# Kernel optimization log

Measured on AMD Instinct MI355X. Metric: run time of the kernel, lower is better.

Reference implementation:

```python
import jax, jax.numpy as jnp
import numpy as np

N, E, R = 100000, 600000, 2      # nodes, edges per relation, relations
IN, H, DH = 128, 8, 16           # input dim, heads, per-head hidden
D = H * DH                       # 128 = hidden_dim * n_heads
RIN, RH = 64, 16                 # relation input / hidden dims
SLOPE = 0.2                      # leaky relu negative slope


def _leaky(v):
    return jnp.where(v >= 0, v, SLOPE * v)


def setup_inputs() -> dict:
    key = jax.random.key(0)
    ks = jax.random.split(key, 18)
    nrm = lambda k, shape, s: jax.random.normal(k, shape, jnp.float32) * s
    sc = 1.0 / np.sqrt(D).astype(np.float32)
    return {
        'x': nrm(ks[0], (N, IN), 1.0),
        'src': jax.random.randint(ks[1], (R, E), 0, N, jnp.int32),
        'dst': jax.random.randint(ks[2], (R, E), 0, N, jnp.int32),
        'rel_emb': nrm(ks[3], (R, RIN), 1.0),
        'Wp': nrm(ks[4], (IN, D), sc), 'bp': jnp.zeros((D,), jnp.float32),
        'Wn': nrm(ks[5], (D, D), sc), 'bn': jnp.zeros((D,), jnp.float32),
        'Wsrc': nrm(ks[6], (R, D, D), sc), 'bsrc': jnp.zeros((R, D), jnp.float32),
        'Wrel': nrm(ks[7], (R, RIN, H * 2 * DH), 1.0 / np.sqrt(RIN).astype(np.float32)),
        'resW': nrm(ks[8], (IN, D), sc), 'resb': jnp.zeros((D,), jnp.float32),
        'res_alpha': nrm(ks[9], (1,), 1.0),
        'crossW': nrm(ks[10], (R, H, DH), 1.0 / np.sqrt(DH).astype(np.float32)),
        'Wprop': nrm(ks[11], (R, RIN, H * RH), 1.0 / np.sqrt(RIN).astype(np.float32)),
        'bprop': jnp.zeros((R, H * RH), jnp.float32),
    }


def reference(x, src, dst, rel_emb, Wp, bp, Wn, bn, Wsrc, bsrc, Wrel,
              resW, resb, res_alpha, crossW, Wprop, bprop):
    # projection_layer (R_HGT) then node_transformation_layers (layer input transform)
    xp = x @ Wp + bp                                  # [N, D]
    h = (xp @ Wn + bn).reshape(N, H, DH)              # [N, H, DH] dst-side features
    res = (xp @ resW + resb).reshape(N, H, DH)        # res_fc(input_dst)

    def per_rel(sr, dr, e_emb, Ws, bs, Wr):
        # relation_src_node_transformation + relation-conditioned attention
        s = (h.reshape(N, D) @ Ws + bs).reshape(N, H, DH)   # src messages
        a = (e_emb @ Wr).reshape(H, 2, DH)                  # relation attn vectors
        sc_src = (s * a[:, 0]).sum(-1)                      # [N, H]
        sc_dst = (h * a[:, 1]).sum(-1)                      # [N, H]
        e_sc = _leaky(sc_src[sr] + sc_dst[dr])              # [E, H]
        # edge softmax over incoming edges of each dst node
        m = jax.lax.stop_gradient(jax.ops.segment_max(e_sc, dr, num_segments=N))
        ex = jnp.exp(e_sc - m[dr])
        den = jax.ops.segment_sum(ex, dr, num_segments=N)
        alpha = ex / den[dr]                                # [E, H]
        msg = alpha[:, :, None] * s[sr]                     # [E, H, DH]
        return jax.ops.segment_sum(msg, dr, num_segments=N)  # [N, H, DH]

    out = jax.vmap(per_rel)(src, dst, rel_emb, Wsrc, bsrc, Wrel)  # [R, N, H, DH]

    # sigmoid-gated residual (shared per dst ntype)
    g = jax.nn.sigmoid(res_alpha)[0]
    out = out * g + res[None] * (1.0 - g)

    # RelationCrossing: attention across the R relation-specific dst features
    def cross(cw):
        attn = jax.nn.softmax(_leaky((out * cw[None, None]).sum(-1)), axis=0)  # [R,N,H]
        return (attn[..., None] * out).sum(0)                                  # [N,H,DH]

    fused = jax.vmap(cross)(crossW).reshape(R, N, D)      # [R, N, D]

    # relation_propagation_layer
    rel_out = jnp.einsum('ri,rio->ro', rel_emb, Wprop) + bprop  # [R, H*RH]
    return fused, rel_out
```

## Files before the change

kernel.cpp:

```cpp
#include <hip/hip_runtime.h>
#include <math.h>

#define NN 100000
#define EE 600000
#define RR 2
#define DD 128
#define HH 8
#define DHH 16
#define RN (RR * NN)
#define NT 26
#define MTOT 6250
#define NB3 ((MTOT + 3) / 4)
#define CHUNK 4096
#define NCH ((EE + CHUNK - 1) / CHUNK)
#define BINW 512
#define NBIN ((NN + BINW - 1) / BINW)
#define BCAPD 4096

typedef unsigned short ushort_t;
typedef short bf16x8 __attribute__((ext_vector_type(8)));
typedef float f32x4 __attribute__((ext_vector_type(4)));
typedef unsigned short u16x4 __attribute__((ext_vector_type(4)));

__device__ __forceinline__ float lrelu(float v) { return v >= 0.f ? v : 0.2f * v; }

__device__ __forceinline__ ushort_t f2bf(float f) {
    unsigned int u = __float_as_uint(f);
    u = (u + 0x7FFFu + ((u >> 16) & 1u)) >> 16;
    return (ushort_t)u;
}
__device__ __forceinline__ float bf2f(ushort_t u) {
    return __uint_as_float(((unsigned int)u) << 16);
}

__global__ __launch_bounds__(128) void k_compose1(
    const float* __restrict__ Wp, const float* __restrict__ bp,
    const float* __restrict__ Wn, const float* __restrict__ bn,
    const float* __restrict__ resW, const float* __restrict__ resb,
    const float* __restrict__ rel_emb, const float* __restrict__ Wrel,
    const float* __restrict__ Wprop, const float* __restrict__ bprop,
    float* __restrict__ Wpn, float* __restrict__ bpn,
    float* __restrict__ Wres_c, float* __restrict__ bres_c,
    float* __restrict__ avec, float* __restrict__ rel_out) {
    __shared__ float row[DD];
    const int rrow = blockIdx.x, tid = threadIdx.x;
    row[tid] = Wp[rrow * DD + tid];
    __syncthreads();
    float acc1 = 0.f, acc2 = 0.f;
    for (int k = 0; k < DD; ++k) {
        float wv = row[k];
        acc1 = fmaf(wv, Wn[k * DD + tid], acc1);
        acc2 = fmaf(wv, resW[k * DD + tid], acc2);
    }
    Wpn[rrow * DD + tid] = acc1;
    Wres_c[rrow * DD + tid] = acc2;
    if (rrow == 0) {
        float b1 = 0.f, b2 = 0.f;
        for (int k = 0; k < DD; ++k) {
            b1 = fmaf(bp[k], Wn[k * DD + tid], b1);
            b2 = fmaf(bp[k], resW[k * DD + tid], b2);
        }
        bpn[tid] = b1 + bn[tid];
        bres_c[tid] = b2 + resb[tid];
    }
    if (rrow < 4) {
        int idx = rrow * DD + tid;
        int r = idx >> 8, o = idx & 255;
        float acc = 0.f;
        for (int i = 0; i < 64; ++i)
            acc += rel_emb[r * 64 + i] * Wrel[(r * 64 + i) * 256 + o];
        avec[idx] = acc;
    } else if (rrow < 6) {
        int o = (rrow - 4) * DD + tid;
        int r = o >> 7, oo = o & 127;
        float acc = bprop[o];
        for (int i = 0; i < 64; ++i)
            acc += rel_emb[r * 64 + i] * Wprop[(r * 64 + i) * 128 + oo];
        rel_out[o] = acc;
    }
}

__global__ __launch_bounds__(128) void k_compose2(
    const float* __restrict__ Wpn, const float* __restrict__ bpn,
    const float* __restrict__ Wsrc, const float* __restrict__ bsrc,
    const float* __restrict__ avec,
    float* __restrict__ Ws_c, float* __restrict__ bs_c,
    float* __restrict__ VdstT, float* __restrict__ cdst) {
    __shared__ float row[DD];
    const int rel = blockIdx.x, rrow = blockIdx.y, tid = threadIdx.x;
    row[tid] = Wpn[rrow * DD + tid];
    __syncthreads();
    const float* W = Wsrc + (size_t)rel * DD * DD;
    float acc = 0.f;
    for (int k = 0; k < DD; ++k) acc = fmaf(row[k], W[k * DD + tid], acc);
    Ws_c[(size_t)rel * DD * DD + rrow * DD + tid] = acc;
    if (tid < HH) {
        float v = 0.f;
        for (int d = 0; d < 16; ++d)
            v += row[tid * 16 + d] * avec[rel * 256 + tid * 32 + 16 + d];
        VdstT[(rel * HH + tid) * DD + rrow] = v;
    }
    if (rrow == 0) {
        float b = 0.f;
        for (int k = 0; k < DD; ++k) b = fmaf(bpn[k], W[k * DD + tid], b);
        bs_c[rel * DD + tid] = b + bsrc[rel * DD + tid];
        if (rel == 0 && tid < 16) {
            int r2 = tid >> 3, h2 = tid & 7;
            float c2 = 0.f;
            for (int d = 0; d < 16; ++d)
                c2 += bpn[h2 * 16 + d] * avec[r2 * 256 + h2 * 32 + 16 + d];
            cdst[tid] = c2;
        }
    }
}

__global__ __launch_bounds__(256) void k_pack(
    const float* __restrict__ Ws_c, const float* __restrict__ Wres_c,
    const float* __restrict__ VdstT, const float* __restrict__ avec,
    const float* __restrict__ bs_c, short* __restrict__ Wpk,
    float* __restrict__ csrc) {
    const int t = blockIdx.x;
    const int kt = threadIdx.x >> 6;
    const int l = threadIdx.x & 63;
    const int c16 = l & 15;
    bf16x8 v;
    #pragma unroll
    for (int j = 0; j < 8; ++j) {
        int k = kt * 32 + (l >> 4) * 8 + j;
        float f;
        if (t < 24) {
            int m = t >> 3;
            int col = (t & 7) * 16 + c16;
            const float* W = (m == 0) ? Ws_c : (m == 1) ? Ws_c + DD * DD : Wres_c;
            f = W[k * DD + col];
        } else if (t == 24) {
            f = VdstT[c16 * DD + k];
        } else {
            int rel = c16 >> 3, h = c16 & 7;
            f = 0.f;
            for (int d = 0; d < 16; ++d)
                f += Ws_c[(size_t)rel * DD * DD + k * DD + h * 16 + d]
                     * avec[rel * 256 + h * 32 + d];
        }
        v[j] = (short)f2bf(f);
    }
    *(bf16x8*)(Wpk + ((size_t)(t * 4 + kt) * 64 + l) * 8) = v;
    if (t == 25 && threadIdx.x < 16) {
        int rel = threadIdx.x >> 3, h = threadIdx.x & 7;
        float c = 0.f;
        for (int d = 0; d < 16; ++d)
            c += bs_c[rel * DD + h * 16 + d] * avec[rel * 256 + h * 32 + d];
        csrc[threadIdx.x] = c;
    }
}

__global__ __launch_bounds__(256) void k_node3(
    const float* __restrict__ x, const short* __restrict__ Wpk,
    const float* __restrict__ bs_c, const float* __restrict__ bres_c,
    const float* __restrict__ cdst, const float* __restrict__ csrc,
    const int* __restrict__ dst, int* __restrict__ binct,
    ushort_t* __restrict__ s_out, ushort_t* __restrict__ res_out,
    float* __restrict__ sc_src, float* __restrict__ sc_dst) {
    if (blockIdx.x >= NB3) {
        __shared__ int bins[NBIN];
        const int b = blockIdx.x - NB3;
        const int rel = b / NCH, blk = b - rel * NCH;
        const int tid = threadIdx.x;
        if (tid < NBIN) bins[tid] = 0;
        __syncthreads();
        for (int i = tid; i < CHUNK; i += 256) {
            int e = blk * CHUNK + i;
            if (e < EE)
                atomicAdd(&bins[__builtin_nontemporal_load(dst + rel * EE + e) >> 9], 1);
        }
        __syncthreads();
        if (tid < NBIN) binct[((rel * NCH) + blk) * NBIN + tid] = bins[tid];
        return;
    }
    const int tid = threadIdx.x;
    const int l = tid & 63;
    const int w = tid >> 6;
    const int m16 = l & 15, g4 = l >> 4;
    const int mt = blockIdx.x * 4 + w;
    const bool live = (mt < MTOT);
    const int nb = (live ? mt : MTOT - 1) * 16;

    bf16x8 af[4];
    const float* xrow = x + (size_t)(nb + m16) * DD + g4 * 8;
    #pragma unroll
    for (int kt = 0; kt < 4; ++kt) {
        float4 v0 = *(const float4*)(xrow + kt * 32);
        float4 v1 = *(const float4*)(xrow + kt * 32 + 4);
        af[kt][0] = (short)f2bf(v0.x); af[kt][1] = (short)f2bf(v0.y);
        af[kt][2] = (short)f2bf(v0.z); af[kt][3] = (short)f2bf(v0.w);
        af[kt][4] = (short)f2bf(v1.x); af[kt][5] = (short)f2bf(v1.y);
        af[kt][6] = (short)f2bf(v1.z); af[kt][7] = (short)f2bf(v1.w);
    }

    for (int t = 0; t < NT; ++t) {
        f32x4 acc = {0.f, 0.f, 0.f, 0.f};
        #pragma unroll
        for (int kt = 0; kt < 4; ++kt) {
            bf16x8 b = *(const bf16x8*)(Wpk + ((size_t)(t * 4 + kt) * 64 + l) * 8);
            acc = __builtin_amdgcn_mfma_f32_16x16x32_bf16(af[kt], b, acc, 0, 0, 0);
        }
        if (!live) continue;
        if (t < 16) {
            const int rel = t >> 3, head = t & 7;
            const float bb = bs_c[rel * DD + head * 16 + m16];
            #pragma unroll
            for (int r = 0; r < 4; ++r) {
                const int node = nb + g4 * 4 + r;
                s_out[((size_t)rel * NN + node) * DD + head * 16 + m16] =
                    f2bf(acc[r] + bb);
            }
        } else if (t < 24) {
            const int col = (t - 16) * 16 + m16;
            const float bb = bres_c[col];
            #pragma unroll
            for (int r = 0; r < 4; ++r) {
                const int node = nb + g4 * 4 + r;
                res_out[(size_t)node * DD + col] = f2bf(acc[r] + bb);
            }
        } else if (t == 24) {
            const int rel = m16 >> 3, head = m16 & 7;
            const float bb = cdst[m16];
            #pragma unroll
            for (int r = 0; r < 4; ++r) {
                const int node = nb + g4 * 4 + r;
                sc_dst[((size_t)rel * NN + node) * HH + head] = acc[r] + bb;
            }
        } else {
            const int rel = m16 >> 3, head = m16 & 7;
            const float bb = csrc[m16];
            #pragma unroll
            for (int r = 0; r < 4; ++r) {
                const int node = nb + g4 * 4 + r;
                sc_src[((size_t)rel * NN + node) * HH + head] = acc[r] + bb;
            }
        }
    }
}

__global__ __launch_bounds__(512) void k_binscan(const int* __restrict__ binct,
                                                 int* __restrict__ runoff,
                                                 int* __restrict__ binstart,
                                                 int* __restrict__ row_ptr) {
    __shared__ int tot[512];
    const int t = threadIdx.x;
    int run = 0;
    if (t < RR * NBIN) {
        const int rel = t / NBIN, bin = t - rel * NBIN;
        for (int blk = 0; blk < NCH; ++blk) {
            int idx = ((rel * NCH) + blk) * NBIN + bin;
            int v = binct[idx];
            runoff[idx] = run;
            run += v;
        }
    }
    tot[t] = (t < RR * NBIN) ? run : 0;
    __syncthreads();
    for (int off = 1; off < 512; off <<= 1) {
        int v = (t >= off) ? tot[t - off] : 0;
        __syncthreads();
        tot[t] += v;
        __syncthreads();
    }
    if (t < RR * NBIN) binstart[t] = tot[t] - run;
    if (t == 0) {
        binstart[RR * NBIN] = RR * EE;
        row_ptr[RN] = RR * EE;
    }
}

__global__ __launch_bounds__(256) void k_binfill(
    const int* __restrict__ src, const int* __restrict__ dst,
    const int* __restrict__ runoff, const int* __restrict__ binstart,
    int* __restrict__ ebuf) {
    __shared__ int ofs[NBIN];
    __shared__ int bins[NBIN];
    const int blk = blockIdx.x, rel = blockIdx.y, tid = threadIdx.x;
    if (tid < NBIN) {
        ofs[tid] = binstart[rel * NBIN + tid] + runoff[((rel * NCH) + blk) * NBIN + tid];
        bins[tid] = 0;
    }
    __syncthreads();
    for (int i = tid; i < CHUNK; i += 256) {
        int e = blk * CHUNK + i;
        if (e < EE) {
            int d = __builtin_nontemporal_load(dst + rel * EE + e);
            int b = d >> 9;
            int loc = atomicAdd(&bins[b], 1);
            ebuf[ofs[b] + loc] =
                ((d & 511) << 17) | __builtin_nontemporal_load(src + rel * EE + e);
        }
    }
}

__global__ __launch_bounds__(256) void k_binfin(
    const int* __restrict__ ebuf, const int* __restrict__ binstart,
    int* __restrict__ row_ptr, int* __restrict__ esrc) {
    __shared__ int keys[BCAPD];
    __shared__ int cnt[BINW];
    __shared__ int scn[BINW];
    __shared__ int part[256];
    const int bin = blockIdx.x, rel = blockIdx.y, tid = threadIdx.x;
    const int p0 = binstart[rel * NBIN + bin];
    const int p1 = binstart[rel * NBIN + bin + 1];
    const int cntE = p1 - p0;
    const bool inlds = (cntE <= BCAPD);
    const int n0 = bin * BINW;
    const int nw = min(BINW, NN - n0);

    cnt[2 * tid] = 0; cnt[2 * tid + 1] = 0;
    __syncthreads();
    for (int i = tid; i < cntE; i += 256) {
        int k = __builtin_nontemporal_load(ebuf + p0 + i);
        if (inlds) keys[i] = k;
        atomicAdd(&cnt[k >> 17], 1);
    }
    __syncthreads();
    int a = cnt[2 * tid], b = cnt[2 * tid + 1];
    part[tid] = a + b;
    __syncthreads();
    for (int off = 1; off < 256; off <<= 1) {
        int v = (tid >= off) ? part[tid - off] : 0;
        __syncthreads();
        part[tid] += v;
        __syncthreads();
    }
    int excl = (tid == 0) ? 0 : part[tid - 1];
    scn[2 * tid] = excl;
    scn[2 * tid + 1] = excl + a;
    cnt[2 * tid] = 0; cnt[2 * tid + 1] = 0;
    __syncthreads();
    for (int n = tid; n < nw; n += 256)
        row_ptr[rel * NN + n0 + n] = p0 + scn[n];
    for (int i = tid; i < cntE; i += 256) {
        int k = inlds ? keys[i] : ebuf[p0 + i];
        int low = k >> 17;
        int slot = atomicAdd(&cnt[low], 1);
        esrc[p0 + scn[low] + slot] = k & 0x1FFFF;
    }
}

__global__ __launch_bounds__(256) void k_gather_cross(
    const int* __restrict__ esrc, const int* __restrict__ row_ptr,
    const float* __restrict__ sc_src, const float* __restrict__ sc_dst,
    const ushort_t* __restrict__ s, const ushort_t* __restrict__ res_buf,
    const float* __restrict__ res_alpha, const float* __restrict__ crossW,
    float* __restrict__ out) {
    int n = blockIdx.x * 4 + (threadIdx.x >> 6);
    if (n >= NN) return;
    const int lane = threadIdx.x & 63;
    const int g = lane >> 5;
    const int j = lane & 31;
    const int h = j >> 2;

    const int seg = g * NN + n;
    const int p0 = row_ptr[seg], p1 = row_ptr[seg + 1];
    const float sd = sc_dst[(size_t)seg * HH + h];

    float den0 = 0.f, den1 = 0.f;
    float4 acc0 = {0.f, 0.f, 0.f, 0.f}, acc1 = {0.f, 0.f, 0.f, 0.f};
    int p = p0;
    for (; p + 1 < p1; p += 2) {
        int sr0 = esrc[p], sr1 = esrc[p + 1];
        ushort4 s40 = *(const ushort4*)(s + (size_t)(g * NN + sr0) * DD + j * 4);
        ushort4 s41 = *(const ushort4*)(s + (size_t)(g * NN + sr1) * DD + j * 4);
        float v0 = lrelu(sc_src[(size_t)(g * NN + sr0) * HH + h] + sd);
        float v1 = lrelu(sc_src[(size_t)(g * NN + sr1) * HH + h] + sd);
        float e0 = __expf(v0);
        float e1 = __expf(v1);
        den0 += e0; den1 += e1;
        acc0.x = fmaf(e0, bf2f(s40.x), acc0.x); acc1.x = fmaf(e1, bf2f(s41.x), acc1.x);
        acc0.y = fmaf(e0, bf2f(s40.y), acc0.y); acc1.y = fmaf(e1, bf2f(s41.y), acc1.y);
        acc0.z = fmaf(e0, bf2f(s40.z), acc0.z); acc1.z = fmaf(e1, bf2f(s41.z), acc1.z);
        acc0.w = fmaf(e0, bf2f(s40.w), acc0.w); acc1.w = fmaf(e1, bf2f(s41.w), acc1.w);
    }
    if (p < p1) {
        int sr0 = esrc[p];
        ushort4 s40 = *(const ushort4*)(s + (size_t)(g * NN + sr0) * DD + j * 4);
        float v0 = lrelu(sc_src[(size_t)(g * NN + sr0) * HH + h] + sd);
        float e0 = __expf(v0);
        den0 += e0;
        acc0.x = fmaf(e0, bf2f(s40.x), acc0.x);
        acc0.y = fmaf(e0, bf2f(s40.y), acc0.y);
        acc0.z = fmaf(e0, bf2f(s40.z), acc0.z);
        acc0.w = fmaf(e0, bf2f(s40.w), acc0.w);
    }
    float den = den0 + den1;
    float4 acc = {acc0.x + acc1.x, acc0.y + acc1.y, acc0.z + acc1.z, acc0.w + acc1.w};
    float inv = (p1 > p0) ? 1.f / den : 0.f;

    float gate = 1.f / (1.f + __expf(-res_alpha[0]));
    u16x4 r4u = __builtin_nontemporal_load(
        (const u16x4*)(res_buf + (size_t)n * DD + j * 4));
    float4 og;
    og.x = fmaf(acc.x * inv, gate, bf2f(r4u[0]) * (1.f - gate));
    og.y = fmaf(acc.y * inv, gate, bf2f(r4u[1]) * (1.f - gate));
    og.z = fmaf(acc.z * inv, gate, bf2f(r4u[2]) * (1.f - gate));
    og.w = fmaf(acc.w * inv, gate, bf2f(r4u[3]) * (1.f - gate));

    float4 oo;
    oo.x = __shfl_xor(og.x, 32);
    oo.y = __shfl_xor(og.y, 32);
    oo.z = __shfl_xor(og.z, 32);
    oo.w = __shfl_xor(og.w, 32);

    float4 cw = *(const float4*)(crossW + g * DD + j * 4);
    float ds_ = og.x * cw.x + og.y * cw.y + og.z * cw.z + og.w * cw.w;
    float do_ = oo.x * cw.x + oo.y * cw.y + oo.z * cw.z + oo.w * cw.w;
    ds_ += __shfl_xor(ds_, 1); ds_ += __shfl_xor(ds_, 2);
    do_ += __shfl_xor(do_, 1); do_ += __shfl_xor(do_, 2);
    float l0 = lrelu(ds_), l1 = lrelu(do_);
    float mm = fmaxf(l0, l1);
    float e0 = __expf(l0 - mm), e1 = __expf(l1 - mm);
    float winv = 1.f / (e0 + e1);
    float w0 = e0 * winv, w1 = e1 * winv;

    f32x4 o;
    o[0] = w0 * og.x + w1 * oo.x;
    o[1] = w0 * og.y + w1 * oo.y;
    o[2] = w0 * og.z + w1 * oo.z;
    o[3] = w0 * og.w + w1 * oo.w;
    __builtin_nontemporal_store(o, (f32x4*)(out + (size_t)(g * NN + n) * DD + j * 4));
}

extern "C" void kernel_launch(void* const* d_in, const int* in_sizes, int n_in,
                              void* d_out, int out_size, void* d_ws, size_t ws_size,
                              hipStream_t stream) {
    const float* x        = (const float*)d_in[0];
    const int*   src      = (const int*)d_in[1];
    const int*   dst      = (const int*)d_in[2];
    const float* rel_emb  = (const float*)d_in[3];
    const float* Wp       = (const float*)d_in[4];
    const float* bp       = (const float*)d_in[5];
    const float* Wn       = (const float*)d_in[6];
    const float* bn       = (const float*)d_in[7];
    const float* Wsrc     = (const float*)d_in[8];
    const float* bsrc     = (const float*)d_in[9];
    const float* Wrel     = (const float*)d_in[10];
    const float* resW     = (const float*)d_in[11];
    const float* resb     = (const float*)d_in[12];
    const float* res_alpha= (const float*)d_in[13];
    const float* crossW   = (const float*)d_in[14];
    const float* Wprop    = (const float*)d_in[15];
    const float* bprop    = (const float*)d_in[16];

    float* out = (float*)d_out;

    ushort_t* s_bf   = (ushort_t*)d_ws;
    ushort_t* res_bf = s_bf + (size_t)RR * NN * DD;
    float* fbase   = (float*)(res_bf + (size_t)NN * DD);
    float* sc_src  = fbase;
    float* sc_dst  = sc_src  + (size_t)RR * NN * HH;
    float* avec    = sc_dst  + (size_t)RR * NN * HH;
    float* Wpn     = avec    + 512;
    float* Wres_c  = Wpn     + DD * DD;
    float* Ws_c    = Wres_c  + DD * DD;
    float* VdstT   = Ws_c    + (size_t)RR * DD * DD;
    float* bpn     = VdstT   + 16 * DD;
    float* bres_c  = bpn     + DD;
    float* bs_c    = bres_c  + DD;
    float* cdst    = bs_c    + RR * DD;
    float* csrc    = cdst    + 16;
    short* Wpk     = (short*)(csrc + 16);
    int*   row_ptr = (int*)(Wpk + (size_t)NT * 4 * 64 * 8);
    int*   binct   = row_ptr + RN + 1;
    int*   runoff  = binct + RR * NCH * NBIN;
    int*   binstart= runoff + RR * NCH * NBIN;
    int*   ebuf    = binstart + RR * NBIN + 1;
    int*   esrc    = ebuf + RR * EE;

    k_compose1<<<DD, DD, 0, stream>>>(Wp, bp, Wn, bn, resW, resb,
                                      rel_emb, Wrel, Wprop, bprop,
                                      Wpn, bpn, Wres_c, bres_c,
                                      avec, out + (size_t)RR * NN * DD);
    k_compose2<<<dim3(RR, DD), DD, 0, stream>>>(Wpn, bpn, Wsrc, bsrc, avec,
                                                Ws_c, bs_c, VdstT, cdst);
    k_pack<<<NT, 256, 0, stream>>>(Ws_c, Wres_c, VdstT, avec, bs_c, Wpk, csrc);
    k_node3<<<NB3 + RR * NCH, 256, 0, stream>>>(
        x, Wpk, bs_c, bres_c, cdst, csrc, dst, binct,
        s_bf, res_bf, sc_src, sc_dst);
    k_binscan<<<1, 512, 0, stream>>>(binct, runoff, binstart, row_ptr);
    k_binfill<<<dim3(NCH, RR), 256, 0, stream>>>(src, dst, runoff, binstart, ebuf);
    k_binfin<<<dim3(NBIN, RR), 256, 0, stream>>>(ebuf, binstart, row_ptr, esrc);
    k_gather_cross<<<(NN + 3) / 4, 256, 0, stream>>>(esrc, row_ptr, sc_src, sc_dst,
                                                     s_bf, res_bf, res_alpha, crossW,
                                                     out);
}
```

Baseline: 209.3 us.

## Fold CSR build stages into weight-composition kernels to overlap and cut launches

Spreads the edge-bucketing pipeline (bin count, bin scan, bin fill, bin finalize) across the existing weight-composition, pack and node-projection kernels as extra blocks. Each CSR stage now runs alongside an independent weight-prep stage, and three kernel launches are removed. The point is to hide the small serial CSR steps behind work that has to happen anyway. In exchange, the bin scan now runs in a single 128-thread block that handles 4 bins per thread. The last binstart entry is no longer written explicitly and relies on the scan writing 4*128 entries, which adds padding assumptions.

```diff
diff --git a/kernel.cpp b/kernel.cpp
--- a/kernel.cpp
+++ b/kernel.cpp
@@ -39,11 +39,29 @@
     const float* __restrict__ resW, const float* __restrict__ resb,
     const float* __restrict__ rel_emb, const float* __restrict__ Wrel,
     const float* __restrict__ Wprop, const float* __restrict__ bprop,
+    const int* __restrict__ dst, int* __restrict__ binct,
     float* __restrict__ Wpn, float* __restrict__ bpn,
     float* __restrict__ Wres_c, float* __restrict__ bres_c,
     float* __restrict__ avec, float* __restrict__ rel_out) {
+    const int tid = threadIdx.x;
+    if (blockIdx.x >= DD) {
+        __shared__ int bins[NBIN];
+        const int b = blockIdx.x - DD;
+        const int rel = b / NCH, blk = b - rel * NCH;
+        for (int i = tid; i < NBIN; i += 128) bins[i] = 0;
+        __syncthreads();
+        for (int i = tid; i < CHUNK; i += 128) {
+            int e = blk * CHUNK + i;
+            if (e < EE)
+                atomicAdd(&bins[__builtin_nontemporal_load(dst + rel * EE + e) >> 9], 1);
+        }
+        __syncthreads();
+        for (int i = tid; i < NBIN; i += 128)
+            binct[((rel * NCH) + blk) * NBIN + i] = bins[i];
+        return;
+    }
     __shared__ float row[DD];
-    const int rrow = blockIdx.x, tid = threadIdx.x;
+    const int rrow = blockIdx.x;
     row[tid] = Wp[rrow * DD + tid];
     __syncthreads();
     float acc1 = 0.f, acc2 = 0.f;
@@ -84,10 +102,48 @@
     const float* __restrict__ Wpn, const float* __restrict__ bpn,
     const float* __restrict__ Wsrc, const float* __restrict__ bsrc,
     const float* __restrict__ avec,
+    const int* __restrict__ binct, int* __restrict__ runoff,
+    int* __restrict__ binstart, int* __restrict__ row_ptr,
     float* __restrict__ Ws_c, float* __restrict__ bs_c,
     float* __restrict__ VdstT, float* __restrict__ cdst) {
+    const int tid = threadIdx.x;
+    if (blockIdx.y == DD) {
+        if (blockIdx.x != 0) return;
+        __shared__ int part[128];
+        int s[4];
+        #pragma unroll
+        for (int q = 0; q < 4; ++q) {
+            int pb = tid * 4 + q;
+            int run = 0;
+            if (pb < RR * NBIN) {
+                int rel = pb / NBIN, bin = pb - rel * NBIN;
+                for (int blk = 0; blk < NCH; ++blk) {
+                    int idx = ((rel * NCH) + blk) * NBIN + bin;
+                    int v = binct[idx];
+                    runoff[idx] = run;
+                    run += v;
+                }
+            }
+            s[q] = run;
+        }
+        part[tid] = s[0] + s[1] + s[2] + s[3];
+        __syncthreads();
+        for (int off = 1; off < 128; off <<= 1) {
+            int v = (tid >= off) ? part[tid - off] : 0;
+            __syncthreads();
+            part[tid] += v;
+            __syncthreads();
+        }
+        int excl = (tid == 0) ? 0 : part[tid - 1];
+        binstart[4 * tid]     = excl;
+        binstart[4 * tid + 1] = excl + s[0];
+        binstart[4 * tid + 2] = excl + s[0] + s[1];
+        binstart[4 * tid + 3] = excl + s[0] + s[1] + s[2];
+        if (tid == 0) row_ptr[RN] = RR * EE;
+        return;
+    }
     __shared__ float row[DD];
-    const int rel = blockIdx.x, rrow = blockIdx.y, tid = threadIdx.x;
+    const int rel = blockIdx.x, rrow = blockIdx.y;
     row[tid] = Wpn[rrow * DD + tid];
     __syncthreads();
     const float* W = Wsrc + (size_t)rel * DD * DD;
@@ -117,11 +173,38 @@
 __global__ __launch_bounds__(256) void k_pack(
     const float* __restrict__ Ws_c, const float* __restrict__ Wres_c,
     const float* __restrict__ VdstT, const float* __restrict__ avec,
-    const float* __restrict__ bs_c, short* __restrict__ Wpk,
-    float* __restrict__ csrc) {
+    const float* __restrict__ bs_c,
+    const int* __restrict__ src, const int* __restrict__ dst,
+    const int* __restrict__ runoff, const int* __restrict__ binstart,
+    int* __restrict__ ebuf,
+    short* __restrict__ Wpk, float* __restrict__ csrc) {
+    const int tid = threadIdx.x;
+    if (blockIdx.x >= NT) {
+        __shared__ int ofs[NBIN];
+        __shared__ int bins[NBIN];
+        const int b = blockIdx.x - NT;
+        const int rel = b / NCH, blk = b - rel * NCH;
+        if (tid < NBIN) {
+            ofs[tid] = binstart[rel * NBIN + tid] +
+                       runoff[((rel * NCH) + blk) * NBIN + tid];
+            bins[tid] = 0;
+        }
+        __syncthreads();
+        for (int i = tid; i < CHUNK; i += 256) {
+            int e = blk * CHUNK + i;
+            if (e < EE) {
+                int d = __builtin_nontemporal_load(dst + rel * EE + e);
+                int bb = d >> 9;
+                int loc = atomicAdd(&bins[bb], 1);
+                ebuf[ofs[bb] + loc] =
+                    ((d & 511) << 17) | __builtin_nontemporal_load(src + rel * EE + e);
+            }
+        }
+        return;
+    }
     const int t = blockIdx.x;
-    const int kt = threadIdx.x >> 6;
-    const int l = threadIdx.x & 63;
+    const int kt = tid >> 6;
+    const int l = tid & 63;
     const int c16 = l & 15;
     bf16x8 v;
     #pragma unroll
@@ -145,12 +228,12 @@
         v[j] = (short)f2bf(f);
     }
     *(bf16x8*)(Wpk + ((size_t)(t * 4 + kt) * 64 + l) * 8) = v;
-    if (t == 25 && threadIdx.x < 16) {
-        int rel = threadIdx.x >> 3, h = threadIdx.x & 7;
+    if (t == 25 && tid < 16) {
+        int rel = tid >> 3, h = tid & 7;
         float c = 0.f;
         for (int d = 0; d < 16; ++d)
             c += bs_c[rel * DD + h * 16 + d] * avec[rel * 256 + h * 32 + d];
-        csrc[threadIdx.x] = c;
+        csrc[tid] = c;
     }
 }
 
@@ -158,26 +241,57 @@
     const float* __restrict__ x, const short* __restrict__ Wpk,
     const float* __restrict__ bs_c, const float* __restrict__ bres_c,
     const float* __restrict__ cdst, const float* __restrict__ csrc,
-    const int* __restrict__ dst, int* __restrict__ binct,
+    const int* __restrict__ ebuf, const int* __restrict__ binstart,
+    int* __restrict__ row_ptr, int* __restrict__ esrc,
     ushort_t* __restrict__ s_out, ushort_t* __restrict__ res_out,
     float* __restrict__ sc_src, float* __restrict__ sc_dst) {
+    const int tid = threadIdx.x;
     if (blockIdx.x >= NB3) {
-        __shared__ int bins[NBIN];
+        __shared__ int keys[BCAPD];
+        __shared__ int cnt[BINW];
+        __shared__ int scn[BINW];
+        __shared__ int part[256];
         const int b = blockIdx.x - NB3;
-        const int rel = b / NCH, blk = b - rel * NCH;
-        const int tid = threadIdx.x;
-        if (tid < NBIN) bins[tid] = 0;
-        __syncthreads();
-        for (int i = tid; i < CHUNK; i += 256) {
-            int e = blk * CHUNK + i;
-            if (e < EE)
-                atomicAdd(&bins[__builtin_nontemporal_load(dst + rel * EE + e) >> 9], 1);
-        }
-        __syncthreads();
-        if (tid < NBIN) binct[((rel * NCH) + blk) * NBIN + tid] = bins[tid];
+        const int rel = b / NBIN, bin = b - rel * NBIN;
+        const int p0 = binstart[rel * NBIN + bin];
+        const int p1 = binstart[rel * NBIN + bin + 1];
+        const int cntE = p1 - p0;
+        const bool inlds = (cntE <= BCAPD);
+        const int n0 = bin * BINW;
+        const int nw = min(BINW, NN - n0);
+
+        cnt[2 * tid] = 0; cnt[2 * tid + 1] = 0;
+        __syncthreads();
+        for (int i = tid; i < cntE; i += 256) {
+            int k = __builtin_nontemporal_load(ebuf + p0 + i);
+            if (inlds) keys[i] = k;
+            atomicAdd(&cnt[k >> 17], 1);
+        }
+        __syncthreads();
+        int a = cnt[2 * tid], c = cnt[2 * tid + 1];
+        part[tid] = a + c;
+        __syncthreads();
+        for (int off = 1; off < 256; off <<= 1) {
+            int v = (tid >= off) ? part[tid - off] : 0;
+            __syncthreads();
+            part[tid] += v;
+            __syncthreads();
+        }
+        int excl = (tid == 0) ? 0 : part[tid - 1];
+        scn[2 * tid] = excl;
+        scn[2 * tid + 1] = excl + a;
+        cnt[2 * tid] = 0; cnt[2 * tid + 1] = 0;
+        __syncthreads();
+        for (int n = tid; n < nw; n += 256)
+            row_ptr[rel * NN + n0 + n] = p0 + scn[n];
+        for (int i = tid; i < cntE; i += 256) {
+            int k = inlds ? keys[i] : ebuf[p0 + i];
+            int low = k >> 17;
+            int slot = atomicAdd(&cnt[low], 1);
+            esrc[p0 + scn[low] + slot] = k & 0x1FFFF;
+        }
         return;
     }
-    const int tid = threadIdx.x;
     const int l = tid & 63;
     const int w = tid >> 6;
     const int m16 = l & 15, g4 = l >> 4;
@@ -242,108 +356,6 @@
     }
 }
 
-__global__ __launch_bounds__(512) void k_binscan(const int* __restrict__ binct,
-                                                 int* __restrict__ runoff,
-                                                 int* __restrict__ binstart,
-                                                 int* __restrict__ row_ptr) {
-    __shared__ int tot[512];
-    const int t = threadIdx.x;
-    int run = 0;
-    if (t < RR * NBIN) {
-        const int rel = t / NBIN, bin = t - rel * NBIN;
-        for (int blk = 0; blk < NCH; ++blk) {
-            int idx = ((rel * NCH) + blk) * NBIN + bin;
-            int v = binct[idx];
-            runoff[idx] = run;
-            run += v;
-        }
-    }
-    tot[t] = (t < RR * NBIN) ? run : 0;
-    __syncthreads();
-    for (int off = 1; off < 512; off <<= 1) {
-        int v = (t >= off) ? tot[t - off] : 0;
-        __syncthreads();
-        tot[t] += v;
-        __syncthreads();
-    }
-    if (t < RR * NBIN) binstart[t] = tot[t] - run;
-    if (t == 0) {
-        binstart[RR * NBIN] = RR * EE;
-        row_ptr[RN] = RR * EE;
-    }
-}
-
-__global__ __launch_bounds__(256) void k_binfill(
-    const int* __restrict__ src, const int* __restrict__ dst,
-    const int* __restrict__ runoff, const int* __restrict__ binstart,
-    int* __restrict__ ebuf) {
-    __shared__ int ofs[NBIN];
-    __shared__ int bins[NBIN];
-    const int blk = blockIdx.x, rel = blockIdx.y, tid = threadIdx.x;
-    if (tid < NBIN) {
-        ofs[tid] = binstart[rel * NBIN + tid] + runoff[((rel * NCH) + blk) * NBIN + tid];
-        bins[tid] = 0;
-    }
-    __syncthreads();
-    for (int i = tid; i < CHUNK; i += 256) {
-        int e = blk * CHUNK + i;
-        if (e < EE) {
-            int d = __builtin_nontemporal_load(dst + rel * EE + e);
-            int b = d >> 9;
-            int loc = atomicAdd(&bins[b], 1);
-            ebuf[ofs[b] + loc] =
-                ((d & 511) << 17) | __builtin_nontemporal_load(src + rel * EE + e);
-        }
-    }
-}
-
-__global__ __launch_bounds__(256) void k_binfin(
-    const int* __restrict__ ebuf, const int* __restrict__ binstart,
-    int* __restrict__ row_ptr, int* __restrict__ esrc) {
-    __shared__ int keys[BCAPD];
-    __shared__ int cnt[BINW];
-    __shared__ int scn[BINW];
-    __shared__ int part[256];
-    const int bin = blockIdx.x, rel = blockIdx.y, tid = threadIdx.x;
-    const int p0 = binstart[rel * NBIN + bin];
-    const int p1 = binstart[rel * NBIN + bin + 1];
-    const int cntE = p1 - p0;
-    const bool inlds = (cntE <= BCAPD);
-    const int n0 = bin * BINW;
-    const int nw = min(BINW, NN - n0);
-
-    cnt[2 * tid] = 0; cnt[2 * tid + 1] = 0;
-    __syncthreads();
-    for (int i = tid; i < cntE; i += 256) {
-        int k = __builtin_nontemporal_load(ebuf + p0 + i);
-        if (inlds) keys[i] = k;
-        atomicAdd(&cnt[k >> 17], 1);
-    }
-    __syncthreads();
-    int a = cnt[2 * tid], b = cnt[2 * tid + 1];
-    part[tid] = a + b;
-    __syncthreads();
-    for (int off = 1; off < 256; off <<= 1) {
-        int v = (tid >= off) ? part[tid - off] : 0;
-        __syncthreads();
-        part[tid] += v;
-        __syncthreads();
-    }
-    int excl = (tid == 0) ? 0 : part[tid - 1];
-    scn[2 * tid] = excl;
-    scn[2 * tid + 1] = excl + a;
-    cnt[2 * tid] = 0; cnt[2 * tid + 1] = 0;
-    __syncthreads();
-    for (int n = tid; n < nw; n += 256)
-        row_ptr[rel * NN + n0 + n] = p0 + scn[n];
-    for (int i = tid; i < cntE; i += 256) {
-        int k = inlds ? keys[i] : ebuf[p0 + i];
-        int low = k >> 17;
-        int slot = atomicAdd(&cnt[low], 1);
-        esrc[p0 + scn[low] + slot] = k & 0x1FFFF;
-    }
-}
-
 __global__ __launch_bounds__(256) void k_gather_cross(
     const int* __restrict__ esrc, const int* __restrict__ row_ptr,
     const float* __restrict__ sc_src, const float* __restrict__ sc_dst,
@@ -470,22 +482,22 @@
     int*   binct   = row_ptr + RN + 1;
     int*   runoff  = binct + RR * NCH * NBIN;
     int*   binstart= runoff + RR * NCH * NBIN;
-    int*   ebuf    = binstart + RR * NBIN + 1;
+    int*   ebuf    = binstart + 520;
     int*   esrc    = ebuf + RR * EE;
 
-    k_compose1<<<DD, DD, 0, stream>>>(Wp, bp, Wn, bn, resW, resb,
-                                      rel_emb, Wrel, Wprop, bprop,
-                                      Wpn, bpn, Wres_c, bres_c,
-                                      avec, out + (size_t)RR * NN * DD);
-    k_compose2<<<dim3(RR, DD), DD, 0, stream>>>(Wpn, bpn, Wsrc, bsrc, avec,
-                                                Ws_c, bs_c, VdstT, cdst);
-    k_pack<<<NT, 256, 0, stream>>>(Ws_c, Wres_c, VdstT, avec, bs_c, Wpk, csrc);
-    k_node3<<<NB3 + RR * NCH, 256, 0, stream>>>(
-        x, Wpk, bs_c, bres_c, cdst, csrc, dst, binct,
+    k_compose1<<<DD + RR * NCH, 128, 0, stream>>>(
+        Wp, bp, Wn, bn, resW, resb, rel_emb, Wrel, Wprop, bprop,
+        dst, binct, Wpn, bpn, Wres_c, bres_c,
+        avec, out + (size_t)RR * NN * DD);
+    k_compose2<<<dim3(RR, DD + 1), 128, 0, stream>>>(
+        Wpn, bpn, Wsrc, bsrc, avec, binct, runoff, binstart, row_ptr,
+        Ws_c, bs_c, VdstT, cdst);
+    k_pack<<<NT + RR * NCH, 256, 0, stream>>>(
+        Ws_c, Wres_c, VdstT, avec, bs_c, src, dst, runoff, binstart, ebuf,
+        Wpk, csrc);
+    k_node3<<<NB3 + RR * NBIN, 256, 0, stream>>>(
+        x, Wpk, bs_c, bres_c, cdst, csrc, ebuf, binstart, row_ptr, esrc,
         s_bf, res_bf, sc_src, sc_dst);
-    k_binscan<<<1, 512, 0, stream>>>(binct, runoff, binstart, row_ptr);
-    k_binfill<<<dim3(NCH, RR), 256, 0, stream>>>(src, dst, runoff, binstart, ebuf);
-    k_binfin<<<dim3(NBIN, RR), 256, 0, stream>>>(ebuf, binstart, row_ptr, esrc);
     k_gather_cross<<<(NN + 3) / 4, 256, 0, stream>>>(esrc, row_ptr, sc_src, sc_dst,
                                                      s_bf, res_bf, res_alpha, crossW,
                                                      out);
```

New measurement: 201.7 us. 3.6% less time.
